# Kernel tuning notes

Measured on AMD Instinct MI355X. Metric: run time of the kernel, lower is better.

## Reference

```python
import jax, jax.numpy as jnp
import numpy as np

T, B, D = 2048, 8, 1024
TINY = float(np.finfo(np.float32).tiny)


def _uniform(k, shape, fan_in):
    b = 1.0 / np.sqrt(fan_in)
    return jax.random.uniform(k, shape, jnp.float32, -b, b)


def setup_inputs() -> dict:
    key = jax.random.key(0)
    ks = jax.random.split(key, 12)
    data = jax.random.normal(ks[0], (T, B, D), jnp.float32)
    return {
        "data": data,
        "qkv_w": _uniform(ks[1], (3 * D, D), D),
        "qkv_b": _uniform(ks[2], (3 * D,), D),
        "pos_bias": jax.random.normal(ks[3], (T, T), jnp.float32) * 0.02,
        "out_w": _uniform(ks[4], (D, D), D),
        "out_b": _uniform(ks[5], (D,), D),
        "fc1_w": _uniform(ks[6], (2 * D, D), D),
        "fc1_b": _uniform(ks[7], (2 * D,), D),
        "fc2_w": _uniform(ks[8], (D, D), D),
        "fc2_b": _uniform(ks[9], (D,), D),
    }


def _layer_norm(x):
    m = jnp.mean(x, axis=-1, keepdims=True)
    v = jnp.mean((x - m) ** 2, axis=-1, keepdims=True)
    return (x - m) / jnp.sqrt(v + TINY)


def _mish(x):
    return x * jnp.tanh(jax.nn.softplus(x))


def reference(data, qkv_w, qkv_b, pos_bias, out_w, out_b, fc1_w, fc1_b, fc2_w, fc2_b):
    # --- AFT branch --- data: [T, B, D]
    h = _layer_norm(data)
    qkv = h @ qkv_w.T + qkv_b                       # [T, B, 3D]
    q, k, v = jnp.split(qkv, 3, axis=-1)
    w = jnp.exp(pos_bias)                           # [T, T]
    ek = jnp.exp(k)                                 # [T, B, D]
    num = jnp.einsum('ij,jbd->ibd', w, ek * v)      # [T, B, D]
    den = jnp.einsum('ij,jbd->ibd', w, ek)
    aft = (jax.nn.sigmoid(q) * (num / den)) @ out_w.T + out_b
    # --- SwiGLU FFN branch ---
    h2 = _layer_norm(data)
    x12 = h2 @ fc1_w.T + fc1_b                      # [T, B, 2D]
    x1, gate = jnp.split(x12, 2, axis=-1)
    ffn = (x1 * _mish(gate)) @ fc2_w.T + fc2_b
    # --- parallel residual sum ---
    return data + aft + ffn
```

## Files before the change

### kernel.cpp

```cpp
#include <hip/hip_runtime.h>
#include <hip/hip_bf16.h>
#include <cmath>
#include <cstdint>

using bf16 = __hip_bfloat16;
typedef __attribute__((ext_vector_type(8))) short short8;
typedef __attribute__((ext_vector_type(4))) float f32x4;
typedef __attribute__((ext_vector_type(4))) unsigned short ushort4v;

#define T_DIM 2048
#define B_DIM 8
#define D_DIM 1024
#define MROWS (T_DIM*B_DIM)
#define N8 (B_DIM*D_DIM)

__device__ __forceinline__ float b2f(bf16 x) { return __bfloat162float(x); }
__device__ __forceinline__ bf16  f2b(float x) { return __float2bfloat16(x); }
__device__ __forceinline__ float us2f(unsigned short u) {
    union { unsigned int i; float f; } x; x.i = ((unsigned int)u) << 16; return x.f;
}
__device__ __forceinline__ unsigned short f2us(float f) {
    bf16 b = __float2bfloat16(f);
    return *(unsigned short*)&b;
}

__device__ __forceinline__ void gload_lds16(const bf16* g, char* l) {
    __builtin_amdgcn_global_load_lds(
        (const __attribute__((address_space(1))) unsigned int*)g,
        (__attribute__((address_space(3))) unsigned int*)l,
        16, 0, 0);
}

__global__ __launch_bounds__(256) void ln_kernel(const float* __restrict__ x,
                                                 bf16* __restrict__ h) {
    const int row = blockIdx.x;
    const int tid = threadIdx.x;
    const float4 v = ((const float4*)(x + (size_t)row * D_DIM))[tid];
    float s1 = v.x + v.y + v.z + v.w;
    float s2 = v.x*v.x + v.y*v.y + v.z*v.z + v.w*v.w;
    #pragma unroll
    for (int off = 32; off > 0; off >>= 1) {
        s1 += __shfl_down(s1, off);
        s2 += __shfl_down(s2, off);
    }
    __shared__ float red[8];
    const int lane = tid & 63, wv = tid >> 6;
    if (lane == 0) { red[wv*2] = s1; red[wv*2+1] = s2; }
    __syncthreads();
    s1 = red[0] + red[2] + red[4] + red[6];
    s2 = red[1] + red[3] + red[5] + red[7];
    const float mean = s1 * (1.0f / D_DIM);
    const float var  = s2 * (1.0f / D_DIM) - mean * mean;
    const float rstd = rsqrtf(var + 1.1754943508222875e-38f);
    bf16* hr = h + (size_t)row * D_DIM + tid * 4;
    hr[0] = f2b((v.x - mean) * rstd);
    hr[1] = f2b((v.y - mean) * rstd);
    hr[2] = f2b((v.z - mean) * rstd);
    hr[3] = f2b((v.w - mean) * rstd);
}

__global__ __launch_bounds__(256) void expw_kernel(const float* __restrict__ p,
                                                   bf16* __restrict__ w, int n4) {
    const int i = blockIdx.x * 256 + threadIdx.x;
    if (i < n4) {
        const float4 v = ((const float4*)p)[i];
        bf16* o = w + (size_t)i * 4;
        o[0] = f2b(expf(v.x)); o[1] = f2b(expf(v.y));
        o[2] = f2b(expf(v.z)); o[3] = f2b(expf(v.w));
    }
}

__global__ __launch_bounds__(256) void cvt_kernel(const float* __restrict__ p,
                                                  bf16* __restrict__ w, int n4) {
    const int i = blockIdx.x * 256 + threadIdx.x;
    if (i < n4) {
        const float4 v = ((const float4*)p)[i];
        bf16* o = w + (size_t)i * 4;
        o[0] = f2b(v.x); o[1] = f2b(v.y); o[2] = f2b(v.z); o[3] = f2b(v.w);
    }
}

__global__ __launch_bounds__(256) void transpose_ekv(
        const unsigned short* __restrict__ ek, const unsigned short* __restrict__ vv,
        unsigned short* __restrict__ EKt, unsigned short* __restrict__ EKVt) {
    __shared__ unsigned short le[64][68];
    __shared__ unsigned short lv[64][68];
    const int t0 = blockIdx.y * 64;
    const int n0 = blockIdx.x * 64;
    const int tid = threadIdx.x;
    const int r = tid >> 4;
    const int c = tid & 15;
    #pragma unroll
    for (int rr = 0; rr < 4; rr++) {
        const int row = rr * 16 + r;
        const size_t gi = (size_t)(t0 + row) * N8 + n0 + c * 4;
        const ushort4v e = *(const ushort4v*)(ek + gi);
        const ushort4v v = *(const ushort4v*)(vv + gi);
        *(ushort4v*)&le[row][c * 4] = e;
        *(ushort4v*)&lv[row][c * 4] = v;
    }
    __syncthreads();
    #pragma unroll
    for (int rr = 0; rr < 4; rr++) {
        const int nrow = rr * 16 + r;
        ushort4v eo, evo;
        #pragma unroll
        for (int j = 0; j < 4; j++) {
            const int tl = c * 4 + j;
            const unsigned short e = le[tl][nrow];
            const unsigned short v = lv[tl][nrow];
            eo[j]  = e;
            evo[j] = f2us(us2f(e) * us2f(v));
        }
        const size_t go = (size_t)(n0 + nrow) * T_DIM + t0 + c * 4;
        *(ushort4v*)(EKt + go)  = eo;
        *(ushort4v*)(EKVt + go) = evo;
    }
}

__global__ __launch_bounds__(256) void attn_combine(
        const unsigned short* __restrict__ C, const unsigned short* __restrict__ sq,
        unsigned short* __restrict__ Y) {
    const size_t i8 = (size_t)blockIdx.x * 256 + threadIdx.x;
    const size_t j0 = i8 * 8;
    const int t = (int)(j0 >> 13);
    const int u = (int)(j0 & 8191);
    const size_t cbase = (size_t)t * 16384 + u;
    const short8 den = *(const short8*)(C + cbase);
    const short8 num = *(const short8*)(C + cbase + 8192);
    const short8 s   = *(const short8*)(sq + j0);
    short8 y;
    #pragma unroll
    for (int j = 0; j < 8; j++) {
        const float n = us2f((unsigned short)num[j]);
        const float d = us2f((unsigned short)den[j]);
        const float sv = us2f((unsigned short)s[j]);
        y[j] = (short)f2us(sv * (n / d));
    }
    *(short8*)(Y + j0) = y;
}

__global__ __launch_bounds__(256) void glu_combine(
        const unsigned short* __restrict__ x12, unsigned short* __restrict__ ffin) {
    const size_t i8 = (size_t)blockIdx.x * 256 + threadIdx.x;
    const size_t j0 = i8 * 8;
    const int row = (int)(j0 >> 10);
    const int d = (int)(j0 & 1023);
    const size_t base = (size_t)row * 2048 + d;
    const short8 x1v = *(const short8*)(x12 + base);
    const short8 gv  = *(const short8*)(x12 + base + 1024);
    short8 o;
    #pragma unroll
    for (int j = 0; j < 8; j++) {
        const float x1 = us2f((unsigned short)x1v[j]);
        const float g  = us2f((unsigned short)gv[j]);
        const float sp = (g > 20.f) ? g : log1pf(expf(g));
        o[j] = (short)f2us(x1 * (g * tanhf(sp)));
    }
    *(short8*)(ffin + j0) = o;
}

enum { EPI_QKV = 0, EPI_BIAS_F32 = 1, EPI_FC2SUM = 2, EPI_STORE_BF16 = 3, EPI_BIAS_BF16 = 4 };

#define BAR() __builtin_amdgcn_s_barrier()

#define RD_A(ABASE, MOFF)                                                       \
    _Pragma("unroll")                                                           \
    for (int m = 0; m < 4; m++) {                                               \
        a[m][0] = *(const short8*)(lds + (ABASE) + (MOFF + m) * 1024);          \
        a[m][1] = *(const short8*)(lds + (ABASE) + (MOFF + m) * 1024 + 8192);   \
    }

#define RD_B(BBASE, NOFF, BREG)                                                 \
    _Pragma("unroll")                                                           \
    for (int n = 0; n < 2; n++) {                                               \
        BREG[n][0] = *(const short8*)(lds + (BBASE) + (NOFF + n) * 1024);       \
        BREG[n][1] = *(const short8*)(lds + (BBASE) + (NOFF + n) * 1024 + 8192);\
    }

#define MFMA_QUAD(MB, NB, BREG)                                               \
    __builtin_amdgcn_s_setprio(1);                                            \
    _Pragma("unroll")                                                         \
    for (int m = 0; m < 4; m++) {                                             \
        _Pragma("unroll")                                                     \
        for (int n = 0; n < 2; n++) {                                         \
            acc[MB + m][NB + n] = __builtin_amdgcn_mfma_f32_16x16x32_bf16(    \
                a[m][0], BREG[n][0], acc[MB + m][NB + n], 0, 0, 0);           \
            acc[MB + m][NB + n] = __builtin_amdgcn_mfma_f32_16x16x32_bf16(    \
                a[m][1], BREG[n][1], acc[MB + m][NB + n], 0, 0, 0);           \
        }                                                                     \
    }                                                                         \
    __builtin_amdgcn_s_setprio(0);

template <int M, int N, int K, int EPI>
__global__ __launch_bounds__(512, 2)
void gemm8(const bf16* __restrict__ A, const bf16* __restrict__ Bt,
           const float* __restrict__ bias,
           void* __restrict__ o0, void* __restrict__ o1, void* __restrict__ o2,
           const float* __restrict__ e1, const float* __restrict__ e2) {
    constexpr int NK = K / 64;
    constexpr int NIT = NK / 2;
    constexpr int KMASK = NK - 1;
    __shared__ char lds[131072];
    const int tid = threadIdx.x;
    const int lane = tid & 63;
    const int wid = tid >> 6;
    const int wr = wid >> 2, wc = wid & 3;
    const int lr = lane & 15;

    const int nwg = gridDim.x * gridDim.y;
    int lin = blockIdx.y * gridDim.x + blockIdx.x;
    lin = (lin & 7) * (nwg >> 3) + (lin >> 3);
    const int bx = lin % gridDim.x, by = lin / gridDim.x;
    const int m0 = by * 256, n0 = bx * 256;

    const int srow  = tid >> 2;
    const int skcol = ((tid & 3) * 8) ^ (((tid >> 5) & 1) << 4);
    const int sdst  = tid * 16;

    const int ck = ((lane >> 4) * 16) ^ (((lane >> 3) & 1) << 5);
    const int abase0 = wr * 16384 + lr * 64 + ck;
    const int abase1 = 65536 + abase0;
    const int bbase0 = 32768 + (wc >> 1) * 16384 + (wc & 1) * 4096 + lr * 64 + ck;
    const int bbase1 = 65536 + bbase0;

    auto STAGE = [&](const bf16* P, int r0, int kt, int ldsoff) {
        const bf16* src = P + (size_t)(r0 + srow) * K + kt + skcol;
        gload_lds16(src,      lds + ldsoff + sdst);
        gload_lds16(src + 32, lds + ldsoff + 8192 + sdst);
    };

    f32x4 acc[8][4] = {};
    short8 a[4][2], blo[2][2], bhi[2][2];

    STAGE(A,  m0,       0, 0);
    STAGE(A,  m0 + 128, 0, 16384);
    STAGE(Bt, n0,       0, 32768);
    STAGE(Bt, n0 + 128, 0, 49152);
    STAGE(Bt, n0,      64, 65536 + 32768);
    STAGE(A,  m0,      64, 65536);
    asm volatile("s_waitcnt vmcnt(4)");
    BAR();

    for (int i = 0; i < NIT; ++i) {
        const int t1k = ((2 * i + 1) & KMASK) * 64;
        const int t2k = ((2 * i + 2) & KMASK) * 64;
        const int t3k = ((2 * i + 3) & KMASK) * 64;
        RD_A(abase0, 0); RD_B(bbase0, 0, blo);
        STAGE(Bt, n0 + 128, t1k, 65536 + 49152);
        BAR(); MFMA_QUAD(0, 0, blo); BAR();
        RD_B(bbase0, 2, bhi);
        STAGE(A, m0 + 128, t1k, 65536 + 16384);
        BAR(); MFMA_QUAD(0, 2, bhi); BAR();
        RD_A(abase0, 4);
        STAGE(Bt, n0, t2k, 32768);
        BAR(); MFMA_QUAD(4, 2, bhi); BAR();
        STAGE(A, m0, t2k, 0);
        asm volatile("s_waitcnt vmcnt(4)");
        BAR(); MFMA_QUAD(4, 0, blo); BAR();
        RD_A(abase1, 0); RD_B(bbase1, 0, blo);
        STAGE(A, m0 + 128, t2k, 16384);
        BAR(); MFMA_QUAD(0, 0, blo); BAR();
        RD_B(bbase1, 2, bhi);
        STAGE(Bt, n0 + 128, t2k, 49152);
        BAR(); MFMA_QUAD(0, 2, bhi); BAR();
        RD_A(abase1, 4);
        STAGE(Bt, n0, t3k, 65536 + 32768);
        BAR(); MFMA_QUAD(4, 2, bhi); BAR();
        STAGE(A, m0, t3k, 65536);
        asm volatile("s_waitcnt vmcnt(4)");
        BAR(); MFMA_QUAD(4, 0, blo); BAR();
    }
    asm volatile("s_waitcnt vmcnt(0)");

    const int rb = (lane >> 4) * 4;
    #pragma unroll
    for (int mm = 0; mm < 8; mm++) {
        #pragma unroll
        for (int nn = 0; nn < 4; nn++) {
            const int col = n0 + wc * 64 + nn * 16 + lr;
            float bv = 0.f;
            if constexpr (EPI != EPI_STORE_BF16) bv = bias[col];
            const int row0 = m0 + wr * 128 + mm * 16 + rb;
            #pragma unroll
            for (int r = 0; r < 4; r++) {
                const int row = row0 + r;
                const float c = acc[mm][nn][r] + bv;
                if constexpr (EPI == EPI_QKV) {
                    const int seg = col >> 10;
                    const int nc = col & 1023;
                    const size_t idx = (size_t)row * 1024 + nc;
                    if (seg == 0)      ((bf16*)o0)[idx] = f2b(1.f / (1.f + expf(-c)));
                    else if (seg == 1) ((bf16*)o1)[idx] = f2b(expf(c));
                    else               ((bf16*)o2)[idx] = f2b(c);
                } else if constexpr (EPI == EPI_BIAS_F32) {
                    ((float*)o0)[(size_t)row * N + col] = c;
                } else if constexpr (EPI == EPI_STORE_BF16 || EPI == EPI_BIAS_BF16) {
                    ((bf16*)o0)[(size_t)row * N + col] = f2b(c);
                } else {
                    const size_t idx = (size_t)row * N + col;
                    ((float*)o0)[idx] = c + e1[idx] + e2[idx];
                }
            }
        }
    }
}

extern "C" void kernel_launch(void* const* d_in, const int* in_sizes, int n_in,
                              void* d_out, int out_size, void* d_ws, size_t ws_size,
                              hipStream_t stream) {
    const float* data  = (const float*)d_in[0];
    const float* qkv_w = (const float*)d_in[1];
    const float* qkv_b = (const float*)d_in[2];
    const float* pos_b = (const float*)d_in[3];
    const float* out_w = (const float*)d_in[4];
    const float* out_b = (const float*)d_in[5];
    const float* fc1_w = (const float*)d_in[6];
    const float* fc1_b = (const float*)d_in[7];
    const float* fc2_w = (const float*)d_in[8];
    const float* fc2_b = (const float*)d_in[9];
    float* out = (float*)d_out;

    char* ws = (char*)d_ws;
    const size_t MB = 1024ull * 1024ull;
    bf16* h    = (bf16*)(ws);
    bf16* Wb   = (bf16*)(ws + 32*MB);
    bf16* sq   = (bf16*)(ws + 40*MB);
    char* slotA = ws + 72*MB;
    char* slotB = ws + 136*MB;
    bf16* qkvw_b = (bf16*)(ws + 200*MB);
    bf16* outw_b = qkvw_b + (size_t)3072 * 1024;
    bf16* fc1w_b = outw_b + (size_t)1024 * 1024;
    bf16* fc2w_b = fc1w_b + (size_t)2048 * 1024;

    bf16* ek   = (bf16*)slotA;
    bf16* vv   = (bf16*)(slotA + 32*MB);
    bf16* EKt  = (bf16*)slotB;
    bf16* EKVt = (bf16*)(slotB + 32*MB);
    bf16* Ccat = (bf16*)slotA;
    bf16* Y    = (bf16*)slotB;
    bf16* x12  = (bf16*)slotA;
    bf16* ffin = (bf16*)(slotB + 32*MB);

    ln_kernel<<<MROWS, 256, 0, stream>>>(data, h);
    expw_kernel<<<4096, 256, 0, stream>>>(pos_b, Wb, T_DIM * T_DIM / 4);
    cvt_kernel<<<3072, 256, 0, stream>>>(qkv_w, qkvw_b, 3072 * 1024 / 4);
    cvt_kernel<<<1024, 256, 0, stream>>>(out_w, outw_b, 1024 * 1024 / 4);
    cvt_kernel<<<2048, 256, 0, stream>>>(fc1_w, fc1w_b, 2048 * 1024 / 4);
    cvt_kernel<<<1024, 256, 0, stream>>>(fc2_w, fc2w_b, 1024 * 1024 / 4);

    gemm8<MROWS, 3072, 1024, EPI_QKV><<<dim3(12, 64), 512, 0, stream>>>(
        h, qkvw_b, qkv_b, sq, ek, vv, nullptr, nullptr);

    transpose_ekv<<<dim3(128, 32), 256, 0, stream>>>(
        (const unsigned short*)ek, (const unsigned short*)vv,
        (unsigned short*)EKt, (unsigned short*)EKVt);

    gemm8<T_DIM, 2 * N8, T_DIM, EPI_STORE_BF16><<<dim3(64, 8), 512, 0, stream>>>(
        Wb, EKt, nullptr, Ccat, nullptr, nullptr, nullptr, nullptr);

    attn_combine<<<8192, 256, 0, stream>>>(
        (const unsigned short*)Ccat, (const unsigned short*)sq, (unsigned short*)Y);

    gemm8<MROWS, 1024, 1024, EPI_BIAS_F32><<<dim3(4, 64), 512, 0, stream>>>(
        Y, outw_b, out_b, out, nullptr, nullptr, nullptr, nullptr);

    gemm8<MROWS, 2048, 1024, EPI_BIAS_BF16><<<dim3(8, 64), 512, 0, stream>>>(
        h, fc1w_b, fc1_b, x12, nullptr, nullptr, nullptr, nullptr);

    glu_combine<<<8192, 256, 0, stream>>>(
        (const unsigned short*)x12, (unsigned short*)ffin);

    gemm8<MROWS, 1024, 1024, EPI_FC2SUM><<<dim3(4, 64), 512, 0, stream>>>(
        ffin, fc2w_b, fc2_b, out, nullptr, nullptr, data, out);
}
```

Measured before the change: 719.7 us.

## Fuse attention divide and SwiGLU gating into GEMM epilogues via interleaved columns

Interleaves den/num columns (EK and EK*V) and the fc1 x1/gate rows so that paired outputs sit in adjacent lanes. The GEMM epilogue then uses a lane shuffle to compute sigmoid(q)*num/den and x1*mish(gate) directly. This removes the separate attn_combine and glu_combine kernels along with the round trip of the wide intermediate tensors through memory. Half the lanes stay idle during stores, and the stores are strided 2-byte writes, which could hurt coalescing.

```diff
diff --git a/kernel.cpp b/kernel.cpp
--- a/kernel.cpp
+++ b/kernel.cpp
@@ -80,9 +80,21 @@
     }
 }
 
+__global__ __launch_bounds__(256) void cvt_ilv_kernel(const float* __restrict__ p,
+                                                      bf16* __restrict__ w) {
+    const int i = blockIdx.x * 256 + threadIdx.x;
+    const size_t j = (size_t)i * 4;
+    const int drow = (int)(j >> 10);
+    const int dcol = (int)(j & 1023);
+    const int srow = (drow >> 1) + (drow & 1) * 1024;
+    const float4 v = *(const float4*)(p + (size_t)srow * 1024 + dcol);
+    bf16* o = w + j;
+    o[0] = f2b(v.x); o[1] = f2b(v.y); o[2] = f2b(v.z); o[3] = f2b(v.w);
+}
+
 __global__ __launch_bounds__(256) void transpose_ekv(
         const unsigned short* __restrict__ ek, const unsigned short* __restrict__ vv,
-        unsigned short* __restrict__ EKt, unsigned short* __restrict__ EKVt) {
+        unsigned short* __restrict__ EKi) {
     __shared__ unsigned short le[64][68];
     __shared__ unsigned short lv[64][68];
     const int t0 = blockIdx.y * 64;
@@ -112,55 +124,14 @@
             eo[j]  = e;
             evo[j] = f2us(us2f(e) * us2f(v));
         }
-        const size_t go = (size_t)(n0 + nrow) * T_DIM + t0 + c * 4;
-        *(ushort4v*)(EKt + go)  = eo;
-        *(ushort4v*)(EKVt + go) = evo;
-    }
-}
-
-__global__ __launch_bounds__(256) void attn_combine(
-        const unsigned short* __restrict__ C, const unsigned short* __restrict__ sq,
-        unsigned short* __restrict__ Y) {
-    const size_t i8 = (size_t)blockIdx.x * 256 + threadIdx.x;
-    const size_t j0 = i8 * 8;
-    const int t = (int)(j0 >> 13);
-    const int u = (int)(j0 & 8191);
-    const size_t cbase = (size_t)t * 16384 + u;
-    const short8 den = *(const short8*)(C + cbase);
-    const short8 num = *(const short8*)(C + cbase + 8192);
-    const short8 s   = *(const short8*)(sq + j0);
-    short8 y;
-    #pragma unroll
-    for (int j = 0; j < 8; j++) {
-        const float n = us2f((unsigned short)num[j]);
-        const float d = us2f((unsigned short)den[j]);
-        const float sv = us2f((unsigned short)s[j]);
-        y[j] = (short)f2us(sv * (n / d));
-    }
-    *(short8*)(Y + j0) = y;
-}
-
-__global__ __launch_bounds__(256) void glu_combine(
-        const unsigned short* __restrict__ x12, unsigned short* __restrict__ ffin) {
-    const size_t i8 = (size_t)blockIdx.x * 256 + threadIdx.x;
-    const size_t j0 = i8 * 8;
-    const int row = (int)(j0 >> 10);
-    const int d = (int)(j0 & 1023);
-    const size_t base = (size_t)row * 2048 + d;
-    const short8 x1v = *(const short8*)(x12 + base);
-    const short8 gv  = *(const short8*)(x12 + base + 1024);
-    short8 o;
-    #pragma unroll
-    for (int j = 0; j < 8; j++) {
-        const float x1 = us2f((unsigned short)x1v[j]);
-        const float g  = us2f((unsigned short)gv[j]);
-        const float sp = (g > 20.f) ? g : log1pf(expf(g));
-        o[j] = (short)f2us(x1 * (g * tanhf(sp)));
-    }
-    *(short8*)(ffin + j0) = o;
-}
-
-enum { EPI_QKV = 0, EPI_BIAS_F32 = 1, EPI_FC2SUM = 2, EPI_STORE_BF16 = 3, EPI_BIAS_BF16 = 4 };
+        const size_t go = (size_t)(2 * (n0 + nrow)) * T_DIM + t0 + c * 4;
+        *(ushort4v*)(EKi + go)         = eo;
+        *(ushort4v*)(EKi + go + T_DIM) = evo;
+    }
+}
+
+enum { EPI_QKV = 0, EPI_BIAS_F32 = 1, EPI_FC2SUM = 2, EPI_STORE_BF16 = 3,
+       EPI_BIAS_BF16 = 4, EPI_ATTN = 5, EPI_GLU = 6 };
 
 #define BAR() __builtin_amdgcn_s_barrier()
 
@@ -280,7 +251,8 @@
         for (int nn = 0; nn < 4; nn++) {
             const int col = n0 + wc * 64 + nn * 16 + lr;
             float bv = 0.f;
-            if constexpr (EPI != EPI_STORE_BF16) bv = bias[col];
+            if constexpr (EPI == EPI_GLU) bv = bias[(col & 1) * 1024 + (col >> 1)];
+            else if constexpr (EPI != EPI_STORE_BF16 && EPI != EPI_ATTN) bv = bias[col];
             const int row0 = m0 + wr * 128 + mm * 16 + rb;
             #pragma unroll
             for (int r = 0; r < 4; r++) {
@@ -297,6 +269,21 @@
                     ((float*)o0)[(size_t)row * N + col] = c;
                 } else if constexpr (EPI == EPI_STORE_BF16 || EPI == EPI_BIAS_BF16) {
                     ((bf16*)o0)[(size_t)row * N + col] = f2b(c);
+                } else if constexpr (EPI == EPI_ATTN) {
+                    const float partner = __shfl_xor(c, 1);
+                    if ((col & 1) == 0) {
+                        const int u = col >> 1;
+                        const float sv = b2f(((const bf16*)e1)[(size_t)row * (N/2) + u]);
+                        ((bf16*)o0)[(size_t)row * (N/2) + u] = f2b(sv * (partner / c));
+                    }
+                } else if constexpr (EPI == EPI_GLU) {
+                    const float partner = __shfl_xor(c, 1);
+                    if ((col & 1) == 0) {
+                        const float g = partner;
+                        const float sp = (g > 20.f) ? g : log1pf(expf(g));
+                        ((bf16*)o0)[(size_t)row * (N/2) + (col >> 1)] =
+                            f2b(c * (g * tanhf(sp)));
+                    }
                 } else {
                     const size_t idx = (size_t)row * N + col;
                     ((float*)o0)[idx] = c + e1[idx] + e2[idx];
@@ -328,25 +315,22 @@
     bf16* sq   = (bf16*)(ws + 40*MB);
     char* slotA = ws + 72*MB;
     char* slotB = ws + 136*MB;
-    bf16* qkvw_b = (bf16*)(ws + 200*MB);
-    bf16* outw_b = qkvw_b + (size_t)3072 * 1024;
-    bf16* fc1w_b = outw_b + (size_t)1024 * 1024;
-    bf16* fc2w_b = fc1w_b + (size_t)2048 * 1024;
+    bf16* qkvw_b  = (bf16*)(ws + 200*MB);
+    bf16* outw_b  = qkvw_b + (size_t)3072 * 1024;
+    bf16* fc1wi_b = outw_b + (size_t)1024 * 1024;
+    bf16* fc2w_b  = fc1wi_b + (size_t)2048 * 1024;
 
     bf16* ek   = (bf16*)slotA;
     bf16* vv   = (bf16*)(slotA + 32*MB);
-    bf16* EKt  = (bf16*)slotB;
-    bf16* EKVt = (bf16*)(slotB + 32*MB);
-    bf16* Ccat = (bf16*)slotA;
-    bf16* Y    = (bf16*)slotB;
-    bf16* x12  = (bf16*)slotA;
-    bf16* ffin = (bf16*)(slotB + 32*MB);
+    bf16* EKi  = (bf16*)slotB;
+    bf16* Y    = (bf16*)slotA;
+    bf16* ffin = (bf16*)slotB;
 
     ln_kernel<<<MROWS, 256, 0, stream>>>(data, h);
     expw_kernel<<<4096, 256, 0, stream>>>(pos_b, Wb, T_DIM * T_DIM / 4);
     cvt_kernel<<<3072, 256, 0, stream>>>(qkv_w, qkvw_b, 3072 * 1024 / 4);
     cvt_kernel<<<1024, 256, 0, stream>>>(out_w, outw_b, 1024 * 1024 / 4);
-    cvt_kernel<<<2048, 256, 0, stream>>>(fc1_w, fc1w_b, 2048 * 1024 / 4);
+    cvt_ilv_kernel<<<2048, 256, 0, stream>>>(fc1_w, fc1wi_b);
     cvt_kernel<<<1024, 256, 0, stream>>>(fc2_w, fc2w_b, 1024 * 1024 / 4);
 
     gemm8<MROWS, 3072, 1024, EPI_QKV><<<dim3(12, 64), 512, 0, stream>>>(
@@ -354,22 +338,16 @@
 
     transpose_ekv<<<dim3(128, 32), 256, 0, stream>>>(
         (const unsigned short*)ek, (const unsigned short*)vv,
-        (unsigned short*)EKt, (unsigned short*)EKVt);
-
-    gemm8<T_DIM, 2 * N8, T_DIM, EPI_STORE_BF16><<<dim3(64, 8), 512, 0, stream>>>(
-        Wb, EKt, nullptr, Ccat, nullptr, nullptr, nullptr, nullptr);
-
-    attn_combine<<<8192, 256, 0, stream>>>(
-        (const unsigned short*)Ccat, (const unsigned short*)sq, (unsigned short*)Y);
+        (unsigned short*)EKi);
+
+    gemm8<T_DIM, 2 * N8, T_DIM, EPI_ATTN><<<dim3(64, 8), 512, 0, stream>>>(
+        Wb, EKi, nullptr, Y, nullptr, nullptr, (const float*)sq, nullptr);
 
     gemm8<MROWS, 1024, 1024, EPI_BIAS_F32><<<dim3(4, 64), 512, 0, stream>>>(
         Y, outw_b, out_b, out, nullptr, nullptr, nullptr, nullptr);
 
-    gemm8<MROWS, 2048, 1024, EPI_BIAS_BF16><<<dim3(8, 64), 512, 0, stream>>>(
-        h, fc1w_b, fc1_b, x12, nullptr, nullptr, nullptr, nullptr);
-
-    glu_combine<<<8192, 256, 0, stream>>>(
-        (const unsigned short*)x12, (unsigned short*)ffin);
+    gemm8<MROWS, 2048, 1024, EPI_GLU><<<dim3(8, 64), 512, 0, stream>>>(
+        h, fc1wi_b, fc1_b, ffin, nullptr, nullptr, nullptr, nullptr);
 
     gemm8<MROWS, 1024, 1024, EPI_FC2SUM><<<dim3(4, 64), 512, 0, stream>>>(
         ffin, fc2w_b, fc2_b, out, nullptr, nullptr, data, out);
```

Result: slower. 793.2 us (+10.2%).
